# Performance work log

Hardware: AMD Instinct MI355X
Metric: run time of the kernel (lower is better)

Reference implementation:

```python
import jax, jax.numpy as jnp
import numpy as np

N = 65536      # nodes in batched graph
E = 2097152    # edges (avg degree 32)
V = 1000       # chord vocabulary size
F_IN = 128     # chord feature dim
H = 256        # hidden_dim
OUT = 128      # out_dim
G = 256        # number of graphs in batch


def _gcn_layer(x, W, b, row, col, norm, n):
    # x: [n, f_in] -> [n, f_out]; PyG GCNConv: linear then normalized aggregation + bias
    x = x @ W
    msg = x[row] * norm[:, None]            # gather at source, scale by sym-norm
    return jax.ops.segment_sum(msg, col, num_segments=n) + b


def setup_inputs() -> dict:
    key = jax.random.key(0)
    ks = jax.random.split(key, 9)
    chord_feats = jax.random.normal(ks[0], (V, F_IN), jnp.float32)
    W1 = jax.random.normal(ks[1], (F_IN, H), jnp.float32) * 0.05
    b1 = jnp.zeros((H,), jnp.float32)
    W2 = jax.random.normal(ks[2], (H, OUT), jnp.float32) * 0.05
    b2 = jnp.zeros((OUT,), jnp.float32)
    edge_attr = jax.random.uniform(ks[3], (E,), jnp.float32)          # positive edge weights
    node_indices = jax.random.randint(ks[4], (N,), 0, V, jnp.int64)
    edge_index = jax.random.randint(ks[5], (2, E), 0, N, jnp.int64)
    batch_index = jnp.sort(jax.random.randint(ks[6], (N,), 0, G, jnp.int64))
    return {"chord_feats": chord_feats, "W1": W1, "b1": b1, "W2": W2, "b2": b2,
            "edge_attr": edge_attr, "node_indices": node_indices,
            "edge_index": edge_index, "batch_index": batch_index}


def reference(chord_feats, W1, b1, W2, b2, edge_attr, node_indices, edge_index, batch_index):
    loops = jnp.arange(N, dtype=edge_index.dtype)
    row = jnp.concatenate([edge_index[0], loops])   # source
    col = jnp.concatenate([edge_index[1], loops])   # target
    ew = jnp.concatenate([edge_attr, jnp.ones((N,), edge_attr.dtype)])  # self-loop weight 1
    # symmetric GCN normalization: D^-1/2 A D^-1/2
    deg = jax.ops.segment_sum(ew, col, num_segments=N)
    dis = jnp.where(deg > 0, jax.lax.rsqrt(jnp.maximum(deg, 1e-30)), 0.0)
    norm = dis[row] * ew * dis[col]

    x = chord_feats[node_indices]                   # [N, F_IN]
    x = jax.nn.relu(_gcn_layer(x, W1, b1, row, col, norm, N))
    x = jax.nn.relu(_gcn_layer(x, W2, b2, row, col, norm, N))

    # global_mean_pool over batch_index
    sums = jax.ops.segment_sum(x, batch_index, num_segments=G)
    counts = jax.ops.segment_sum(jnp.ones((N,), x.dtype), batch_index, num_segments=G)
    return sums / jnp.maximum(counts, 1.0)[:, None]
```

## Files before the change

### kernel.cpp

```cpp
#include <hip/hip_runtime.h>
#include <hip/hip_fp16.h>
#include <math.h>

constexpr int N_NODES = 65536;
constexpr int N_EDGES = 2097152;
constexpr int F_IN    = 128;
constexpr int H_DIM   = 256;
constexpr int O_DIM   = 128;
constexpr int N_GRAPH = 256;
constexpr int V_SIZE  = 1000;

constexpr int EPB  = 8192;
constexpr int NBLK = N_EDGES / EPB;
constexpr float FXP = 16777216.0f;

typedef _Float16 half8 __attribute__((ext_vector_type(8)));
typedef float floatx4 __attribute__((ext_vector_type(4)));


__global__ void k_init(float* __restrict__ pool, const int* __restrict__ batch,
                       float* __restrict__ cntf, const float* __restrict__ cf,
                       const float* __restrict__ W1, __half* __restrict__ cfW1,
                       const float* __restrict__ W2, _Float16* __restrict__ W2T) {
    __shared__ float xs[8 * F_IN];
    int i = blockIdx.x * blockDim.x + threadIdx.x;
    if (i < N_GRAPH * O_DIM) pool[i] = 0.0f;
    if (blockIdx.x == 0) {
        int g = threadIdx.x;
        int lo = 0, hi = N_NODES;
        while (lo < hi) { int m = (lo + hi) >> 1; if (batch[m] < g) lo = m + 1; else hi = m; }
        int start = lo;
        lo = 0; hi = N_NODES;
        while (lo < hi) { int m = (lo + hi) >> 1; if (batch[m] <= g) lo = m + 1; else hi = m; }
        cntf[g] = (float)(lo - start);
    }
    if (blockIdx.x < V_SIZE / 8) {
        int rb = blockIdx.x * 8;
        int t  = threadIdx.x;
        #pragma unroll
        for (int p = 0; p < 4; ++p) {
            int idx = p * 256 + t;
            int r = idx >> 7, k = idx & 127;
            xs[idx] = cf[(size_t)(rb + r) * F_IN + k];
        }
        __syncthreads();
        float acc[8] = {};
        for (int k = 0; k < F_IN; ++k) {
            float w = W1[k * H_DIM + t];
            #pragma unroll
            for (int j = 0; j < 8; ++j) acc[j] += xs[j * F_IN + k] * w;
        }
        #pragma unroll
        for (int j = 0; j < 8; ++j)
            cfW1[(size_t)(rb + j) * H_DIM + t] = __float2half(acc[j]);
    }
    if (blockIdx.x >= 128) {
        int idx = (blockIdx.x - 128) * 256 + threadIdx.x;
        int nn = idx >> 8, kk = idx & 255;
        W2T[idx] = (_Float16)W2[kk * O_DIM + nn];
    }
}


__global__ void k_hist(const int* __restrict__ col, int* __restrict__ hist) {
    __shared__ int h[256];
    int t = threadIdx.x;
    h[t] = 0;
    __syncthreads();
    int base = blockIdx.x * EPB;
    #pragma unroll
    for (int i = 0; i < EPB / 256; ++i)
        atomicAdd(&h[col[base + i * 256 + t] >> 8], 1);
    __syncthreads();
    hist[t * NBLK + blockIdx.x] = h[t];
}


__global__ void k_scan1(const int* __restrict__ in, int* __restrict__ out,
                        int* __restrict__ bsum) {
    __shared__ int s[256];
    int tid = threadIdx.x;
    int i = blockIdx.x * 256 + tid;
    int v = in[i];
    s[tid] = v;
    __syncthreads();
    for (int d = 1; d < 256; d <<= 1) {
        int t = (tid >= d) ? s[tid - d] : 0;
        __syncthreads();
        s[tid] += t;
        __syncthreads();
    }
    out[i] = s[tid] - v;
    if (tid == 255) bsum[blockIdx.x] = s[255];
}

__global__ void k_scan2(int* __restrict__ bsum) {
    __shared__ int s[256];
    int tid = threadIdx.x;
    int v = bsum[tid];
    s[tid] = v;
    __syncthreads();
    for (int d = 1; d < 256; d <<= 1) {
        int t = (tid >= d) ? s[tid - d] : 0;
        __syncthreads();
        s[tid] += t;
        __syncthreads();
    }
    bsum[tid] = s[tid] - v;
}


__global__ void k_part(const int* __restrict__ row, const int* __restrict__ col,
                       const float* __restrict__ ew, const int* __restrict__ nidx,
                       const int* __restrict__ hoffs, const int* __restrict__ bsum,
                       int2* __restrict__ part) {
    __shared__ int cur[256];
    int t = threadIdx.x;
    cur[t] = hoffs[t * NBLK + blockIdx.x] + bsum[t];
    __syncthreads();
    int base = blockIdx.x * EPB;
    for (int i = 0; i < EPB / 256; ++i) {
        int e = base + i * 256 + t;
        int r = row[e], c = col[e];
        unsigned hw = (unsigned)__half_as_ushort(__float2half(ew[e]));
        int vb = nidx[r];
        int slot = atomicAdd(&cur[c >> 8], 1);
        int2 rec;
        rec.x = (r << 16) | ((c & 255) << 8) | (vb >> 2);
        rec.y = (int)(((unsigned)(vb & 3) << 16) | hw);
        part[slot] = rec;
    }
}


__global__ void k_build1(const int* __restrict__ hoffs, const int* __restrict__ bsum,
                         const int2* __restrict__ part, float* __restrict__ dis,
                         int* __restrict__ offs) {
    __shared__ unsigned long long dc[256];
    __shared__ int sc[256];
    int t = threadIdx.x;
    int bucket = blockIdx.x;
    dc[t] = 0ULL;
    __syncthreads();
    int start = hoffs[bucket * NBLK] + bsum[bucket];
    int end   = (bucket == 255) ? N_EDGES : (hoffs[(bucket + 1) * NBLK] + bsum[bucket + 1]);
    for (int j = start + t; j < end; j += 256) {
        int2 rec = part[j];
        int dst = (rec.x >> 8) & 255;
        float w = __half2float(__ushort_as_half((unsigned short)(rec.y & 0xFFFF)));
        atomicAdd(&dc[dst], (1ULL << 40) |
                  (unsigned long long)(unsigned)(w * FXP + 0.5f));
    }
    __syncthreads();
    unsigned long long v = dc[t];
    float deg = 1.0f + (float)(v & 0xFFFFFFFFFFULL) * (1.0f / FXP);
    dis[bucket * 256 + t] = 1.0f / sqrtf(deg);
    int cnt = (int)(v >> 40);
    sc[t] = cnt;
    __syncthreads();
    for (int d = 1; d < 256; d <<= 1) {
        int x = (t >= d) ? sc[t - d] : 0;
        __syncthreads();
        sc[t] += x;
        __syncthreads();
    }
    offs[bucket * 256 + t] = start + sc[t] - cnt;
    if (bucket == 255 && t == 255) offs[N_NODES] = N_EDGES;
}


__global__ void k_build2(const int* __restrict__ hoffs, const int* __restrict__ bsum,
                         const int2* __restrict__ part, const float* __restrict__ dis,
                         const int* __restrict__ offs, int2* __restrict__ csr) {
    __shared__ int cur[256];
    int t = threadIdx.x;
    int bucket = blockIdx.x;
    cur[t] = offs[bucket * 256 + t];
    __syncthreads();
    int start = hoffs[bucket * NBLK] + bsum[bucket];
    int end   = (bucket == 255) ? N_EDGES : (hoffs[(bucket + 1) * NBLK] + bsum[bucket + 1]);
    for (int j = start + t; j < end; j += 256) {
        int2 rec = part[j];
        int dst = (rec.x >> 8) & 255;
        unsigned src = ((unsigned)rec.x) >> 16;
        int vb = ((rec.x & 255) << 2) | ((rec.y >> 16) & 3);
        float w = __half2float(__ushort_as_half((unsigned short)(rec.y & 0xFFFF)));
        float nm = dis[src] * w;
        int slot = atomicAdd(&cur[dst], 1);
        int2 e;
        e.x = (int)((src << 10) | (unsigned)vb);
        e.y = __float_as_int(nm);
        csr[slot] = e;
    }
}


__global__ void k_agg1(const int2* __restrict__ cfW1, const int* __restrict__ nidx,
                       const float* __restrict__ dis, const int* __restrict__ offs,
                       const int2* __restrict__ csr, const float4* __restrict__ b1f4,
                       int2* __restrict__ h1) {
    int wave = threadIdx.x >> 6;
    int lane = threadIdx.x & 63;
    int c = blockIdx.x * 4 + wave;
    float d = dis[c];
    int2 sp = cfW1[(size_t)nidx[c] * 64 + lane];
    float2 sa = __half22float2(*(__half2*)&sp.x);
    float2 sb = __half22float2(*(__half2*)&sp.y);
    float4 esum = {0.f, 0.f, 0.f, 0.f};
    int a0 = offs[c], a1 = offs[c + 1];
    int s = a0;
    for (; s + 8 <= a1; s += 8) {
        int sb_i = __builtin_amdgcn_readfirstlane(s);
        int2 e[8];
        #pragma unroll
        for (int u = 0; u < 8; ++u) e[u] = csr[sb_i + u];
        int2 v[8];
        #pragma unroll
        for (int u = 0; u < 8; ++u)
            v[u] = cfW1[(size_t)(e[u].x & 1023) * 64 + lane];
        #pragma unroll
        for (int u = 0; u < 8; ++u) {
            float n = __int_as_float(e[u].y);
            float2 va = __half22float2(*(__half2*)&v[u].x);
            float2 vb = __half22float2(*(__half2*)&v[u].y);
            esum.x += va.x * n; esum.y += va.y * n;
            esum.z += vb.x * n; esum.w += vb.y * n;
        }
    }
    for (; s < a1; ++s) {
        int sb_i = __builtin_amdgcn_readfirstlane(s);
        int2 e0 = csr[sb_i];
        int2 v0 = cfW1[(size_t)(e0.x & 1023) * 64 + lane];
        float n = __int_as_float(e0.y);
        float2 va = __half22float2(*(__half2*)&v0.x);
        float2 vb = __half22float2(*(__half2*)&v0.y);
        esum.x += va.x * n; esum.y += va.y * n;
        esum.z += vb.x * n; esum.w += vb.y * n;
    }
    float4 bb = b1f4[lane];
    float dd = d * d;
    float r0 = bb.x + sa.x * dd + d * esum.x;
    float r1 = bb.y + sa.y * dd + d * esum.y;
    float r2 = bb.z + sb.x * dd + d * esum.z;
    float r3 = bb.w + sb.y * dd + d * esum.w;
    r0 = r0 > 0.f ? r0 : 0.f;  r1 = r1 > 0.f ? r1 : 0.f;
    r2 = r2 > 0.f ? r2 : 0.f;  r3 = r3 > 0.f ? r3 : 0.f;
    float2 p0 = {r0, r1}, p1 = {r2, r3};
    __half2 ha = __float22half2_rn(p0);
    __half2 hb = __float22half2_rn(p1);
    int2 outv;
    outv.x = *(int*)&ha;
    outv.y = *(int*)&hb;
    h1[(size_t)c * 64 + lane] = outv;
}


__global__ void k_gemm2(const _Float16* __restrict__ h1, const _Float16* __restrict__ W2T,
                        __half* __restrict__ xw2h) {
    int wave = threadIdx.x >> 6;
    int lane = threadIdx.x & 63;
    int quad = lane >> 4;
    int n    = lane & 15;
    int tm   = blockIdx.x * 4 + wave;
    const _Float16* arow = h1 + (size_t)(tm * 16 + n) * H_DIM;
    half8 a[8];
    #pragma unroll
    for (int kt = 0; kt < 8; ++kt)
        a[kt] = *(const half8*)(arow + kt * 32 + quad * 8);
    #pragma unroll
    for (int nt = 0; nt < 8; ++nt) {
        floatx4 acc = {0.f, 0.f, 0.f, 0.f};
        const _Float16* brow = W2T + (size_t)(nt * 16 + n) * H_DIM;
        #pragma unroll
        for (int kt = 0; kt < 8; ++kt) {
            half8 b = *(const half8*)(brow + kt * 32 + quad * 8);
            acc = __builtin_amdgcn_mfma_f32_16x16x32_f16(a[kt], b, acc, 0, 0, 0);
        }
        #pragma unroll
        for (int r = 0; r < 4; ++r) {
            int rowi = tm * 16 + quad * 4 + r;
            xw2h[(size_t)rowi * O_DIM + nt * 16 + n] = __float2half(acc[r]);
        }
    }
}


__global__ void k_agg2_pool(const __half2* __restrict__ xw2h, const float* __restrict__ b2,
                            const float* __restrict__ dis, const int* __restrict__ offs,
                            const int2* __restrict__ csr, const int* __restrict__ batch,
                            float* __restrict__ pool) {
    __shared__ float2 red[4][64];
    __shared__ int bgs[4];
    int wave = threadIdx.x >> 6;
    int lane = threadIdx.x & 63;
    int c = blockIdx.x * 4 + wave;
    float d = dis[c];
    float2 self = __half22float2(xw2h[(size_t)c * 64 + lane]);
    float2 bb = ((const float2*)b2)[lane];
    float2 esum = {0.f, 0.f};
    int s0 = offs[c], s1 = offs[c + 1];
    int s = s0;
    for (; s + 8 <= s1; s += 8) {
        int sb_i = __builtin_amdgcn_readfirstlane(s);
        int2 e[8];
        #pragma unroll
        for (int u = 0; u < 8; ++u) e[u] = csr[sb_i + u];
        float2 v[8];
        #pragma unroll
        for (int u = 0; u < 8; ++u)
            v[u] = __half22float2(xw2h[(size_t)(e[u].x >> 10) * 64 + lane]);
        #pragma unroll
        for (int u = 0; u < 8; ++u) {
            float n = __int_as_float(e[u].y);
            esum.x += v[u].x * n; esum.y += v[u].y * n;
        }
    }
    for (; s < s1; ++s) {
        int sb_i = __builtin_amdgcn_readfirstlane(s);
        int2 e0 = csr[sb_i];
        float2 v0 = __half22float2(xw2h[(size_t)(e0.x >> 10) * 64 + lane]);
        float n0 = __int_as_float(e0.y);
        esum.x += v0.x * n0; esum.y += v0.y * n0;
    }
    float dd = d * d;
    float2 acc;
    acc.x = bb.x + self.x * dd + d * esum.x;
    acc.y = bb.y + self.y * dd + d * esum.y;
    acc.x = acc.x > 0.0f ? acc.x : 0.0f;
    acc.y = acc.y > 0.0f ? acc.y : 0.0f;
    red[wave][lane] = acc;
    if (lane == 0) bgs[wave] = batch[c];
    __syncthreads();
    if (wave == 0) {
        float2 a = red[0][lane];
        int cg = bgs[0];
        #pragma unroll
        for (int w = 1; w < 4; ++w) {
            int g = bgs[w];
            float2 r = red[w][lane];
            if (g == cg) { a.x += r.x; a.y += r.y; }
            else {
                atomicAdd(&pool[cg * O_DIM + 2 * lane], a.x);
                atomicAdd(&pool[cg * O_DIM + 2 * lane + 1], a.y);
                a = r; cg = g;
            }
        }
        atomicAdd(&pool[cg * O_DIM + 2 * lane], a.x);
        atomicAdd(&pool[cg * O_DIM + 2 * lane + 1], a.y);
    }
}

__global__ void k_final(const float* __restrict__ pool, const float* __restrict__ cnt,
                        float* __restrict__ out) {
    int t = blockIdx.x * blockDim.x + threadIdx.x;
    if (t < N_GRAPH * O_DIM) {
        int g = t / O_DIM;
        out[t] = pool[t] / fmaxf(cnt[g], 1.0f);
    }
}


extern "C" void kernel_launch(void* const* d_in, const int* in_sizes, int n_in,
                              void* d_out, int out_size, void* d_ws, size_t ws_size,
                              hipStream_t stream) {
    const float* cf   = (const float*)d_in[0];
    const float* W1   = (const float*)d_in[1];
    const float* b1   = (const float*)d_in[2];
    const float* W2   = (const float*)d_in[3];
    const float* b2   = (const float*)d_in[4];
    const float* ew   = (const float*)d_in[5];
    const int*   nidx = (const int*)d_in[6];
    const int*   eidx = (const int*)d_in[7];
    const int*   bidx = (const int*)d_in[8];
    float* out = (float*)d_out;

    const int* row = eidx;
    const int* col = eidx + N_EDGES;

    char* ws = (char*)d_ws;
    size_t off = 0;
    int*   hist  = (int*)  (ws + off); off += (size_t)N_NODES * 4;
    int*   hoffs = (int*)  (ws + off); off += (size_t)N_NODES * 4;
    int*   bsum  = (int*)  (ws + off); off += 4096;
    float* dis   = (float*)(ws + off); off += (size_t)N_NODES * 4;
    int*   offs  = (int*)  (ws + off); off += (size_t)(N_NODES + 16) * 4;
    int2*  csr   = (int2*) (ws + off); off += (size_t)N_EDGES * 8;
    float* pool  = (float*)(ws + off); off += (size_t)(N_GRAPH * O_DIM + N_GRAPH) * 4;
    __half* cfW1 = (__half*)(ws + off); off += (size_t)V_SIZE * H_DIM * 2;
    _Float16* W2T = (_Float16*)(ws + off); off += (size_t)O_DIM * H_DIM * 2;
    off = (off + 255) & ~(size_t)255;
    int2*  part  = (int2*) (ws + off); off += (size_t)N_EDGES * 8;
    __half* h1   = (__half*)(ws + off);
    __half* xw2h = (__half*)part;
    float* cntf  = pool + N_GRAPH * O_DIM;

    k_init<<<256, 256, 0, stream>>>(pool, bidx, cntf, cf, W1, cfW1, W2, W2T);
    k_hist<<<NBLK, 256, 0, stream>>>(col, hist);
    k_scan1<<<256, 256, 0, stream>>>(hist, hoffs, bsum);
    k_scan2<<<1, 256, 0, stream>>>(bsum);

    k_part<<<NBLK, 256, 0, stream>>>(row, col, ew, nidx, hoffs, bsum, part);
    k_build1<<<256, 256, 0, stream>>>(hoffs, bsum, part, dis, offs);
    k_build2<<<256, 256, 0, stream>>>(hoffs, bsum, part, dis, offs, csr);

    k_agg1<<<N_NODES / 4, 256, 0, stream>>>((const int2*)cfW1, nidx, dis, offs, csr,
                                            (const float4*)b1, (int2*)h1);

    k_gemm2<<<N_NODES / 64, 256, 0, stream>>>((const _Float16*)h1, W2T, xw2h);
    k_agg2_pool<<<N_NODES / 4, 256, 0, stream>>>((const __half2*)xw2h, b2, dis, offs, csr,
                                                 bidx, pool);

    k_final<<<(N_GRAPH * O_DIM + 255) / 256, 256, 0, stream>>>(pool, cntf, out);
}
```

Measured before the change: 346.8 us.

## Fuse histogram into init, merge scan passes, cache bucket records in LDS

Folds the column histogram into the init kernel and merges the two scan kernels using a last-block atomic counter, so the chain issues two fewer launches. The build stage is reorganised: a separate degree kernel computes dis first. A combined build kernel then stages each bucket's records in shared memory, recomputes degrees and offsets, and emits the CSR without a second global read of part. In exchange it adds a large shared-memory footprint that lowers occupancy. It also computes dis redundantly, and one block rewrites dis with identical values while other blocks read the same array through a restrict-qualified alias.

```diff
diff --git a/kernel.cpp b/kernel.cpp
--- a/kernel.cpp
+++ b/kernel.cpp
@@ -12,6 +12,7 @@
 
 constexpr int EPB  = 8192;
 constexpr int NBLK = N_EDGES / EPB;
+constexpr int BCAP = 9216;
 constexpr float FXP = 16777216.0f;
 
 typedef _Float16 half8 __attribute__((ext_vector_type(8)));
@@ -21,12 +22,23 @@
 __global__ void k_init(float* __restrict__ pool, const int* __restrict__ batch,
                        float* __restrict__ cntf, const float* __restrict__ cf,
                        const float* __restrict__ W1, __half* __restrict__ cfW1,
-                       const float* __restrict__ W2, _Float16* __restrict__ W2T) {
+                       const float* __restrict__ W2, _Float16* __restrict__ W2T,
+                       const int* __restrict__ col, int* __restrict__ hist,
+                       int* __restrict__ scnt) {
     __shared__ float xs[8 * F_IN];
-    int i = blockIdx.x * blockDim.x + threadIdx.x;
+    __shared__ int h[256];
+    int t = threadIdx.x;
+    int i = blockIdx.x * blockDim.x + t;
     if (i < N_GRAPH * O_DIM) pool[i] = 0.0f;
+    if (i == 0) *scnt = 0;
+    h[t] = 0;
+    __syncthreads();
+    int base = blockIdx.x * EPB;
+    #pragma unroll
+    for (int p = 0; p < EPB / 256; ++p)
+        atomicAdd(&h[col[base + p * 256 + t] >> 8], 1);
     if (blockIdx.x == 0) {
-        int g = threadIdx.x;
+        int g = t;
         int lo = 0, hi = N_NODES;
         while (lo < hi) { int m = (lo + hi) >> 1; if (batch[m] < g) lo = m + 1; else hi = m; }
         int start = lo;
@@ -36,7 +48,6 @@
     }
     if (blockIdx.x < V_SIZE / 8) {
         int rb = blockIdx.x * 8;
-        int t  = threadIdx.x;
         #pragma unroll
         for (int p = 0; p < 4; ++p) {
             int idx = p * 256 + t;
@@ -55,30 +66,19 @@
             cfW1[(size_t)(rb + j) * H_DIM + t] = __float2half(acc[j]);
     }
     if (blockIdx.x >= 128) {
-        int idx = (blockIdx.x - 128) * 256 + threadIdx.x;
+        int idx = (blockIdx.x - 128) * 256 + t;
         int nn = idx >> 8, kk = idx & 255;
         W2T[idx] = (_Float16)W2[kk * O_DIM + nn];
     }
-}
-
-
-__global__ void k_hist(const int* __restrict__ col, int* __restrict__ hist) {
-    __shared__ int h[256];
-    int t = threadIdx.x;
-    h[t] = 0;
-    __syncthreads();
-    int base = blockIdx.x * EPB;
-    #pragma unroll
-    for (int i = 0; i < EPB / 256; ++i)
-        atomicAdd(&h[col[base + i * 256 + t] >> 8], 1);
     __syncthreads();
     hist[t * NBLK + blockIdx.x] = h[t];
 }
 
 
-__global__ void k_scan1(const int* __restrict__ in, int* __restrict__ out,
-                        int* __restrict__ bsum) {
+__global__ void k_scan(const int* __restrict__ in, int* __restrict__ out,
+                       int* __restrict__ bsum, int* __restrict__ scnt) {
     __shared__ int s[256];
+    __shared__ int lastFlag;
     int tid = threadIdx.x;
     int i = blockIdx.x * 256 + tid;
     int v = in[i];
@@ -92,21 +92,22 @@
     }
     out[i] = s[tid] - v;
     if (tid == 255) bsum[blockIdx.x] = s[255];
-}
-
-__global__ void k_scan2(int* __restrict__ bsum) {
-    __shared__ int s[256];
-    int tid = threadIdx.x;
-    int v = bsum[tid];
-    s[tid] = v;
-    __syncthreads();
-    for (int d = 1; d < 256; d <<= 1) {
-        int t = (tid >= d) ? s[tid - d] : 0;
-        __syncthreads();
-        s[tid] += t;
-        __syncthreads();
-    }
-    bsum[tid] = s[tid] - v;
+    __threadfence();
+    if (tid == 0) lastFlag = (atomicAdd(scnt, 1) == 255) ? 1 : 0;
+    __syncthreads();
+    if (lastFlag) {
+        __threadfence();
+        int bv = bsum[tid];
+        s[tid] = bv;
+        __syncthreads();
+        for (int d = 1; d < 256; d <<= 1) {
+            int t = (tid >= d) ? s[tid - d] : 0;
+            __syncthreads();
+            s[tid] += t;
+            __syncthreads();
+        }
+        bsum[tid] = s[tid] - bv;
+    }
 }
 
 
@@ -133,11 +134,66 @@
 }
 
 
-__global__ void k_build1(const int* __restrict__ hoffs, const int* __restrict__ bsum,
-                         const int2* __restrict__ part, float* __restrict__ dis,
-                         int* __restrict__ offs) {
+__global__ void k_build(const int* __restrict__ hoffs, const int* __restrict__ bsum,
+                        const int2* __restrict__ part, const float* __restrict__ dis_in,
+                        float* __restrict__ dis, int* __restrict__ offs,
+                        int2* __restrict__ csr) {
+    __shared__ int2 recs[BCAP];
     __shared__ unsigned long long dc[256];
     __shared__ int sc[256];
+    __shared__ int cur[256];
+    int t = threadIdx.x;
+    int bucket = blockIdx.x;
+    dc[t] = 0ULL;
+    __syncthreads();
+    int start = hoffs[bucket * NBLK] + bsum[bucket];
+    int end   = (bucket == 255) ? N_EDGES : (hoffs[(bucket + 1) * NBLK] + bsum[bucket + 1]);
+    int n = end - start;
+    for (int j = t; j < n; j += 256) {
+        int2 rec = part[start + j];
+        if (j < BCAP) recs[j] = rec;
+        int dst = (rec.x >> 8) & 255;
+        float w = __half2float(__ushort_as_half((unsigned short)(rec.y & 0xFFFF)));
+        atomicAdd(&dc[dst], (1ULL << 40) |
+                  (unsigned long long)(unsigned)(w * FXP + 0.5f));
+    }
+    __syncthreads();
+    unsigned long long v = dc[t];
+    float deg = 1.0f + (float)(v & 0xFFFFFFFFFFULL) * (1.0f / FXP);
+    dis[bucket * 256 + t] = 1.0f / sqrtf(deg);
+    int cnt = (int)(v >> 40);
+    sc[t] = cnt;
+    __syncthreads();
+    for (int d = 1; d < 256; d <<= 1) {
+        int x = (t >= d) ? sc[t - d] : 0;
+        __syncthreads();
+        sc[t] += x;
+        __syncthreads();
+    }
+    int node_off = start + sc[t] - cnt;
+    offs[bucket * 256 + t] = node_off;
+    cur[t] = node_off;
+    if (bucket == 255 && t == 255) offs[N_NODES] = N_EDGES;
+    __syncthreads();
+    for (int j = t; j < n; j += 256) {
+        int2 rec = (j < BCAP) ? recs[j] : part[start + j];
+        int dst = (rec.x >> 8) & 255;
+        unsigned src = ((unsigned)rec.x) >> 16;
+        int vb = ((rec.x & 255) << 2) | ((rec.y >> 16) & 3);
+        float w = __half2float(__ushort_as_half((unsigned short)(rec.y & 0xFFFF)));
+        float nm = dis_in[src] * w;
+        int slot = atomicAdd(&cur[dst], 1);
+        int2 e;
+        e.x = (int)((src << 10) | (unsigned)vb);
+        e.y = __float_as_int(nm);
+        csr[slot] = e;
+    }
+}
+
+
+__global__ void k_deg(const int* __restrict__ hoffs, const int* __restrict__ bsum,
+                      const int2* __restrict__ part, float* __restrict__ dis) {
+    __shared__ unsigned long long dc[256];
     int t = threadIdx.x;
     int bucket = blockIdx.x;
     dc[t] = 0ULL;
@@ -155,43 +211,6 @@
     unsigned long long v = dc[t];
     float deg = 1.0f + (float)(v & 0xFFFFFFFFFFULL) * (1.0f / FXP);
     dis[bucket * 256 + t] = 1.0f / sqrtf(deg);
-    int cnt = (int)(v >> 40);
-    sc[t] = cnt;
-    __syncthreads();
-    for (int d = 1; d < 256; d <<= 1) {
-        int x = (t >= d) ? sc[t - d] : 0;
-        __syncthreads();
-        sc[t] += x;
-        __syncthreads();
-    }
-    offs[bucket * 256 + t] = start + sc[t] - cnt;
-    if (bucket == 255 && t == 255) offs[N_NODES] = N_EDGES;
-}
-
-
-__global__ void k_build2(const int* __restrict__ hoffs, const int* __restrict__ bsum,
-                         const int2* __restrict__ part, const float* __restrict__ dis,
-                         const int* __restrict__ offs, int2* __restrict__ csr) {
-    __shared__ int cur[256];
-    int t = threadIdx.x;
-    int bucket = blockIdx.x;
-    cur[t] = offs[bucket * 256 + t];
-    __syncthreads();
-    int start = hoffs[bucket * NBLK] + bsum[bucket];
-    int end   = (bucket == 255) ? N_EDGES : (hoffs[(bucket + 1) * NBLK] + bsum[bucket + 1]);
-    for (int j = start + t; j < end; j += 256) {
-        int2 rec = part[j];
-        int dst = (rec.x >> 8) & 255;
-        unsigned src = ((unsigned)rec.x) >> 16;
-        int vb = ((rec.x & 255) << 2) | ((rec.y >> 16) & 3);
-        float w = __half2float(__ushort_as_half((unsigned short)(rec.y & 0xFFFF)));
-        float nm = dis[src] * w;
-        int slot = atomicAdd(&cur[dst], 1);
-        int2 e;
-        e.x = (int)((src << 10) | (unsigned)vb);
-        e.y = __float_as_int(nm);
-        csr[slot] = e;
-    }
 }
 
 
@@ -382,6 +401,7 @@
     int*   hist  = (int*)  (ws + off); off += (size_t)N_NODES * 4;
     int*   hoffs = (int*)  (ws + off); off += (size_t)N_NODES * 4;
     int*   bsum  = (int*)  (ws + off); off += 4096;
+    int*   scnt  = (int*)  (ws + off); off += 256;
     float* dis   = (float*)(ws + off); off += (size_t)N_NODES * 4;
     int*   offs  = (int*)  (ws + off); off += (size_t)(N_NODES + 16) * 4;
     int2*  csr   = (int2*) (ws + off); off += (size_t)N_EDGES * 8;
@@ -394,14 +414,13 @@
     __half* xw2h = (__half*)part;
     float* cntf  = pool + N_GRAPH * O_DIM;
 
-    k_init<<<256, 256, 0, stream>>>(pool, bidx, cntf, cf, W1, cfW1, W2, W2T);
-    k_hist<<<NBLK, 256, 0, stream>>>(col, hist);
-    k_scan1<<<256, 256, 0, stream>>>(hist, hoffs, bsum);
-    k_scan2<<<1, 256, 0, stream>>>(bsum);
+    k_init<<<256, 256, 0, stream>>>(pool, bidx, cntf, cf, W1, cfW1, W2, W2T,
+                                    col, hist, scnt);
+    k_scan<<<256, 256, 0, stream>>>(hist, hoffs, bsum, scnt);
 
     k_part<<<NBLK, 256, 0, stream>>>(row, col, ew, nidx, hoffs, bsum, part);
-    k_build1<<<256, 256, 0, stream>>>(hoffs, bsum, part, dis, offs);
-    k_build2<<<256, 256, 0, stream>>>(hoffs, bsum, part, dis, offs, csr);
+    k_deg<<<256, 256, 0, stream>>>(hoffs, bsum, part, dis);
+    k_build<<<256, 256, 0, stream>>>(hoffs, bsum, part, dis, dis, offs, csr);
 
     k_agg1<<<N_NODES / 4, 256, 0, stream>>>((const int2*)cfW1, nidx, dis, offs, csr,
                                             (const float4*)b1, (int2*)h1);
```

After: 369.7 us. 1.07x slower.
